# Optimization experiments

Measured on AMD Instinct MI355X. Metric: run time of the kernel, lower is better.

Reference implementation:

```python
import jax, jax.numpy as jnp
import numpy as np

H = 64            # hidden_channels
L = 2             # num_layers
E = 300_000       # edges per relation
B = 64            # graphs in batch
NS = [100_000, 20_000, 50_000, 80_000]   # variable, value, operator, constraint
# (src_type, dst_type) for the 9 hetero relations, fixed order
RELS = [(0,1),(0,2),(0,3),(2,3),(3,3),(1,0),(2,0),(3,0),(3,2)]
R = len(RELS)
SLOPE = 0.2       # GATConv leaky_relu negative slope


def setup_inputs() -> dict:
    key = jax.random.key(0)
    ks = iter(jax.random.split(key, 64))
    inp = {}
    for n, N in zip(["x_variable", "x_value", "x_operator", "x_constraint"], NS):
        inp[n] = jax.random.normal(next(ks), (N, H), jnp.float32)
    sc = 1.0 / np.sqrt(H).astype(np.float32)
    inp["Wsrc"] = jax.random.normal(next(ks), (L, R, H, H), jnp.float32) * sc
    inp["Wdst"] = jax.random.normal(next(ks), (L, R, H, H), jnp.float32) * sc
    inp["asrc"] = jax.random.normal(next(ks), (L, R, H), jnp.float32) * sc
    inp["adst"] = jax.random.normal(next(ks), (L, R, H), jnp.float32) * sc
    inp["bias"] = jax.random.normal(next(ks), (L, R, H), jnp.float32) * 0.01
    inp["lin_w"] = jax.random.normal(next(ks), (2, 2 * H), jnp.float32) / np.sqrt(2.0 * H).astype(np.float32)
    inp["lin_b"] = jnp.zeros((2,), jnp.float32)
    for r, (s, d) in enumerate(RELS):
        inp[f"src{r}"] = jax.random.randint(next(ks), (E,), 0, NS[s], jnp.int32)
        inp[f"dst{r}"] = jax.random.randint(next(ks), (E,), 0, NS[d], jnp.int32)
    inp["batch_variable"] = jnp.sort(jax.random.randint(next(ks), (NS[0],), 0, B, jnp.int32))
    inp["batch_constraint"] = jnp.sort(jax.random.randint(next(ks), (NS[3],), 0, B, jnp.int32))
    inp["num_graphs"] = B
    return inp


def _gat(xs, xd, Ws, Wd, a_s, a_d, b, src, dst):
    """Bipartite PyG GATConv (heads=1, add_self_loops=False)."""
    hs = xs @ Ws                         # [Ns, H]
    hd = xd @ Wd                         # [Nd, H]
    al_s = hs @ a_s                      # [Ns]
    al_d = hd @ a_d                      # [Nd]
    score = jax.nn.leaky_relu(al_s[src] + al_d[dst], SLOPE)    # [E]
    nd = xd.shape[0]
    m = jax.ops.segment_max(score, dst, num_segments=nd)
    p = jnp.exp(score - m[dst])
    z = jax.ops.segment_sum(p, dst, num_segments=nd)
    alpha = p / (z[dst] + 1e-16)                               # segment softmax
    out = jax.ops.segment_sum(hs[src] * alpha[:, None], dst, num_segments=nd)
    return out + b


def _seg_mean(x, seg, n):
    s = jax.ops.segment_sum(x, seg, num_segments=n)
    c = jax.ops.segment_sum(jnp.ones((x.shape[0],), x.dtype), seg, num_segments=n)
    return s / jnp.maximum(c, 1.0)[:, None]


def reference(x_variable, x_value, x_operator, x_constraint,
              Wsrc, Wdst, asrc, adst, bias, lin_w, lin_b,
              src0, dst0, src1, dst1, src2, dst2, src3, dst3, src4, dst4,
              src5, dst5, src6, dst6, src7, dst7, src8, dst8,
              batch_variable, batch_constraint, num_graphs):
    xs = [x_variable, x_value, x_operator, x_constraint]
    srcs = [src0, src1, src2, src3, src4, src5, src6, src7, src8]
    dsts = [dst0, dst1, dst2, dst3, dst4, dst5, dst6, dst7, dst8]
    for l in range(L):
        out = [jnp.zeros((x.shape[0], H), x.dtype) for x in xs]
        for r, (s, d) in enumerate(RELS):
            out[d] = out[d] + _gat(xs[s], xs[d], Wsrc[l, r], Wdst[l, r],
                                   asrc[l, r], adst[l, r], bias[l, r],
                                   srcs[r], dsts[r])
        xs = [jax.nn.relu(o) for o in out]   # dropout is identity in eval
    vp = _seg_mean(xs[0], batch_variable, num_graphs)   # [B, H]
    cp = _seg_mean(xs[3], batch_constraint, num_graphs) # [B, H]
    return jnp.concatenate([vp, cp], axis=1) @ lin_w.T + lin_b   # [B, 2]
```

## Files before the change

### kernel.cpp

```cpp
#include <hip/hip_runtime.h>
#include <hip/hip_bf16.h>

#define NH 64
#define NRELS 9
#define NEDGE 300000
#define NGRAPH 64
#define TOTROWS 250000
#define TOTFSEG 660000
#define TOTEDGE (NRELS * NEDGE)
#define NBUCK 977
#define CHUNK 4096
#define NBLK ((TOTEDGE + CHUNK - 1) / CHUNK)

typedef __attribute__((ext_vector_type(8))) short short8;
typedef __attribute__((ext_vector_type(4))) float f32x4;

__constant__ int c_NS[4]     = {100000, 20000, 50000, 80000};
__constant__ int c_SRC[9]    = {0,0,0,2,3,1,2,3,3};
__constant__ int c_DST[9]    = {1,2,3,3,3,0,0,0,2};
__constant__ int c_XOFF[5]   = {0,100000,120000,170000,250000};
__constant__ int c_ASOFF[10] = {0,100000,200000,300000,350000,430000,450000,500000,580000,660000};
__constant__ int c_FOFF[5]   = {0,300000,320000,420000,660000};
__constant__ int c_NRELT[4]  = {3,1,2,3};
__constant__ int c_RRANK[9]  = {0,0,0,1,2,0,1,2,1};

struct EdgePtrs { const int* s[9]; const int* d[9]; };

__device__ __forceinline__ unsigned short f2bf(float f) {
  union { __hip_bfloat16 h; unsigned short u; } c;
  c.h = __float2bfloat16(f);
  return c.u;
}

__device__ __forceinline__ float wred_max32(float v) {
#pragma unroll
  for (int o = 16; o; o >>= 1) v = fmaxf(v, __shfl_xor(v, o, 32));
  return v;
}

__global__ void k_setup(const float* Wsrc, const float* Wdst, const float* asrc,
                        const float* adst, const float* bias, float* wv, float* bsum,
                        unsigned short* wb, int* gbh) {
  int b = blockIdx.x, j = threadIdx.x;
  if (b < 36) {
    int r = b % 9, q = b / 9;
    int l = q >> 1, side = q & 1;
    const float* W = (side ? Wdst : Wsrc) + (l * 9 + r) * 64 * 64;
    const float* a = (side ? adst : asrc) + (l * 9 + r) * 64;
    float s = 0.f;
    for (int i = 0; i < 64; ++i) s += W[j * 64 + i] * a[i];
    wv[(side ? 1152 : 0) + (l * 9 + r) * 64 + j] = s;
  } else if (b == 36) {
    for (int l = 0; l < 2; ++l)
      for (int t = 0; t < 4; ++t) {
        float s = 0.f;
        for (int r = 0; r < 9; ++r)
          if (c_DST[r] == t) s += bias[(l * 9 + r) * 64 + j];
        bsum[(l * 4 + t) * 64 + j] = s;
      }
  } else if (b == 55) {
    for (int i = j; i < NBUCK; i += 64) gbh[i] = 0;
  } else {
    int idx = b - 37;
    int l = idx / 9, r = idx % 9;
    const float* W = Wsrc + (size_t)(l * 9 + r) * 4096;
    unsigned short* dst = wb + (size_t)(l * 9 + r) * 4096;
    for (int k = 0; k < 64; ++k)
      dst[j * 64 + k] = f2bf(W[k * 64 + j]);
  }
}

__global__ __launch_bounds__(256) void k_bhist(EdgePtrs Eg, int* gbh) {
  __shared__ int sh[NBUCK];
  for (int i = threadIdx.x; i < NBUCK; i += 256) sh[i] = 0;
  __syncthreads();
  int lo = blockIdx.x * CHUNK;
  int hi = lo + CHUNK; if (hi > TOTEDGE) hi = TOTEDGE;
  for (int gid = lo + threadIdx.x; gid < hi; gid += 256) {
    int r = gid / NEDGE, e = gid - r * NEDGE;
    int g = c_XOFF[c_DST[r]] + Eg.d[r][e];
    atomicAdd(&sh[g >> 8], 1);
  }
  __syncthreads();
  for (int i = threadIdx.x; i < NBUCK; i += 256) {
    int v = sh[i];
    if (v) atomicAdd(&gbh[i], v);
  }
}

__global__ void k_bscan(const int* gbh, int* boff, int* cur) {
  __shared__ int sd[1024];
  int t = threadIdx.x;
  int v = (t < NBUCK) ? gbh[t] : 0;
  sd[t] = v; __syncthreads();
  for (int o = 1; o < 1024; o <<= 1) {
    int x = (t >= o) ? sd[t - o] : 0; __syncthreads();
    sd[t] += x; __syncthreads();
  }
  if (t < NBUCK) { int e = sd[t] - v; boff[t] = e; cur[t] = e; }
  if (t == 1023) boff[NBUCK] = sd[1023];
}

__global__ __launch_bounds__(256) void k_bin(EdgePtrs Eg, int* cur, int* pairs) {
  __shared__ int sh[NBUCK];
  __shared__ int sbase[NBUCK];
  for (int i = threadIdx.x; i < NBUCK; i += 256) sh[i] = 0;
  __syncthreads();
  int lo = blockIdx.x * CHUNK;
  int hi = lo + CHUNK; if (hi > TOTEDGE) hi = TOTEDGE;
  for (int gid = lo + threadIdx.x; gid < hi; gid += 256) {
    int r = gid / NEDGE, e = gid - r * NEDGE;
    int g = c_XOFF[c_DST[r]] + Eg.d[r][e];
    atomicAdd(&sh[g >> 8], 1);
  }
  __syncthreads();
  for (int i = threadIdx.x; i < NBUCK; i += 256) {
    int v = sh[i];
    sbase[i] = v ? atomicAdd(&cur[i], v) : 0;
    sh[i] = 0;
  }
  __syncthreads();
  for (int gid = lo + threadIdx.x; gid < hi; gid += 256) {
    int r = gid / NEDGE, e = gid - r * NEDGE;
    int g = c_XOFF[c_DST[r]] + Eg.d[r][e];
    int b = g >> 8;
    int off = atomicAdd(&sh[b], 1);
    int key = ((g & 255) << 2) | c_RRANK[r];
    pairs[sbase[b] + off] = (key << 20) | (c_ASOFF[r] + Eg.s[r][e]);
  }
}

__global__ __launch_bounds__(256) void k_bsort(const int* pairs, const int* boff,
                                               int* rowptr, int* asx) {
  __shared__ int ssc[1024];
  __shared__ int scur[1024];
  __shared__ int sws[256];
  int b = blockIdx.x, t = threadIdx.x;
  int lo = boff[b], hi = boff[b + 1];
  int n = hi - lo;
  for (int i = t; i < 1024; i += 256) ssc[i] = 0;
  __syncthreads();
  for (int i = t; i < n; i += 256)
    atomicAdd(&ssc[((unsigned)pairs[lo + i]) >> 20], 1);
  __syncthreads();
  int c0 = ssc[t * 4], c1 = ssc[t * 4 + 1], c2 = ssc[t * 4 + 2], c3 = ssc[t * 4 + 3];
  int s = c0 + c1 + c2 + c3;
  sws[t] = s;
  __syncthreads();
  for (int o = 1; o < 256; o <<= 1) {
    int x = (t >= o) ? sws[t - o] : 0; __syncthreads();
    sws[t] += x; __syncthreads();
  }
  int base = sws[t] - s;
  ssc[t * 4]     = base;
  ssc[t * 4 + 1] = base + c0;
  ssc[t * 4 + 2] = base + c0 + c1;
  ssc[t * 4 + 3] = base + c0 + c1 + c2;
  scur[t * 4]     = ssc[t * 4];
  scur[t * 4 + 1] = ssc[t * 4 + 1];
  scur[t * 4 + 2] = ssc[t * 4 + 2];
  scur[t * 4 + 3] = ssc[t * 4 + 3];
  __syncthreads();
  int nodeBase = b << 8;
  for (int i = t; i < 1024; i += 256) {
    int l = i >> 2, rank = i & 3;
    int g = nodeBase + l;
    if (g < TOTROWS) {
      int tt = (g >= c_XOFF[1]) + (g >= c_XOFF[2]) + (g >= c_XOFF[3]);
      int nr = c_NRELT[tt];
      if (rank < nr)
        rowptr[c_FOFF[tt] + (g - c_XOFF[tt]) * nr + rank] = lo + ssc[i];
    }
  }
  if (b == 0 && t == 0) rowptr[TOTFSEG] = TOTEDGE;
  for (int i = t; i < n; i += 256) {
    int p = pairs[lo + i];
    int pos = atomicAdd(&scur[((unsigned)p) >> 20], 1);
    asx[lo + pos] = (int)(((((unsigned)p >> 20) & 3u) << 20) | ((unsigned)p & 0xFFFFFu));
  }
}

struct GemmAllP {
  const float* x0; const float* x1; const float* x2; const float* x3;
  const unsigned short* Wb;
  __hip_bfloat16* hs;
  float* als; float* ald;
  const float* wvs; const float* wvd;
  int act; int ntyp;
  int tbase[5];
  int typ[4];
  int nrel[4];
  int rel[4][3];
  int ndrel[4];
  int drel[4][3];
};

#define XSTR 72

__global__ __launch_bounds__(256) void k_gemma(GemmAllP G) {
  __shared__ unsigned short sx[64 * XSTR];
  __shared__ unsigned short sw[64 * XSTR];
  int bid = blockIdx.x;
  int k = 0;
#pragma unroll 3
  for (int q = 1; q < 4; ++q) if (q < G.ntyp) k += (bid >= G.tbase[q]);
  int st = G.typ[k];
  int tile = bid - G.tbase[k];
  int Ns = c_NS[st];
  const float* x = st == 0 ? G.x0 : st == 1 ? G.x1 : st == 2 ? G.x2 : G.x3;
  int base = tile * 64;
  int tid = threadIdx.x;
  for (int kk = tid; kk < 1024; kk += 256) {
    int row = kk >> 4;
    int c4 = (kk & 15) * 4;
    int gr = base + row;
    float4 v = make_float4(0.f, 0.f, 0.f, 0.f);
    if (gr < Ns) v = ((const float4*)x)[(size_t)gr * 16 + (kk & 15)];
    if (G.act) { v.x = fmaxf(v.x, 0.f); v.y = fmaxf(v.y, 0.f); v.z = fmaxf(v.z, 0.f); v.w = fmaxf(v.w, 0.f); }
    ushort4 u;
    u.x = f2bf(v.x); u.y = f2bf(v.y); u.z = f2bf(v.z); u.w = f2bf(v.w);
    *(ushort4*)&sx[row * XSTR + c4] = u;
  }
  __syncthreads();
  {
    int row = tid >> 2, part = tid & 3;
    int gr2 = base + row;
    if (gr2 < Ns) {
      float xv[16];
      const float4* xr = (const float4*)x + (size_t)gr2 * 16 + part * 4;
      float4 v0 = xr[0], v1 = xr[1], v2 = xr[2], v3 = xr[3];
      xv[0]=v0.x; xv[1]=v0.y; xv[2]=v0.z; xv[3]=v0.w;
      xv[4]=v1.x; xv[5]=v1.y; xv[6]=v1.z; xv[7]=v1.w;
      xv[8]=v2.x; xv[9]=v2.y; xv[10]=v2.z; xv[11]=v2.w;
      xv[12]=v3.x; xv[13]=v3.y; xv[14]=v3.z; xv[15]=v3.w;
      if (G.act) {
#pragma unroll
        for (int i = 0; i < 16; ++i) xv[i] = fmaxf(xv[i], 0.f);
      }
      int nrl0 = G.nrel[k];
      for (int ri = 0; ri < nrl0; ++ri) {
        int r = G.rel[k][ri];
        const float* wvp = G.wvs + r * 64 + part * 16;
        float s = 0.f;
#pragma unroll
        for (int i = 0; i < 16; ++i) s += xv[i] * wvp[i];
        s += __shfl_xor(s, 1);
        s += __shfl_xor(s, 2);
        if (part == 0) G.als[c_ASOFF[r] + gr2] = s;
      }
      int ndl = G.ndrel[k];
      for (int ri = 0; ri < ndl; ++ri) {
        int r = G.drel[k][ri];
        const float* wvp = G.wvd + r * 64 + part * 16;
        float s = 0.f;
#pragma unroll
        for (int i = 0; i < 16; ++i) s += xv[i] * wvp[i];
        s += __shfl_xor(s, 1);
        s += __shfl_xor(s, 2);
        if (part == 0)
          G.ald[c_FOFF[st] + gr2 * c_NRELT[st] + c_RRANK[r]] = s;
      }
    }
  }
  int w    = tid >> 6;
  int lane = tid & 63;
  int m    = lane & 15;
  int quad = lane >> 4;
  short8 a0 = *(const short8*)&sx[(w * 16 + m) * XSTR + quad * 8];
  short8 a1 = *(const short8*)&sx[(w * 16 + m) * XSTR + 32 + quad * 8];
  int nrl = G.nrel[k];
  for (int ri = 0; ri < nrl; ++ri) {
    int r = G.rel[k][ri];
    const unsigned short* Wb = G.Wb + (size_t)r * 4096;
    if (ri) __syncthreads();
    {
      int n = tid >> 2;
      int k0 = (tid & 3) << 4;
      short8 w0 = *(const short8*)&Wb[n * 64 + k0];
      short8 w1 = *(const short8*)&Wb[n * 64 + k0 + 8];
      *(short8*)&sw[n * XSTR + k0] = w0;
      *(short8*)&sw[n * XSTR + k0 + 8] = w1;
    }
    __syncthreads();
    f32x4 acc[4];
#pragma unroll
    for (int cb = 0; cb < 4; ++cb) acc[cb] = (f32x4)(0.f);
#pragma unroll
    for (int cb = 0; cb < 4; ++cb) {
      short8 b0 = *(const short8*)&sw[(cb * 16 + m) * XSTR + quad * 8];
      short8 b1 = *(const short8*)&sw[(cb * 16 + m) * XSTR + 32 + quad * 8];
      acc[cb] = __builtin_amdgcn_mfma_f32_16x16x32_bf16(a0, b0, acc[cb], 0, 0, 0);
      acc[cb] = __builtin_amdgcn_mfma_f32_16x16x32_bf16(a1, b1, acc[cb], 0, 0, 0);
    }
    __hip_bfloat16* hsb = G.hs + (size_t)c_ASOFF[r] * 64;
#pragma unroll
    for (int cb = 0; cb < 4; ++cb)
#pragma unroll
      for (int reg = 0; reg < 4; ++reg)
        sx[(w * 16 + quad * 4 + reg) * XSTR + cb * 16 + m] = f2bf(acc[cb][reg]);
    int rrow = w * 16 + (lane >> 2);
    int rcol = (lane & 3) * 16;
    int lr = base + rrow;
    if (lr < Ns) {
      short8 v0 = *(const short8*)&sx[rrow * XSTR + rcol];
      short8 v1 = *(const short8*)&sx[rrow * XSTR + rcol + 8];
      *(short8*)&hsb[(size_t)lr * 64 + rcol] = v0;
      *(short8*)&hsb[(size_t)lr * 64 + rcol + 8] = v1;
    }
  }
}

struct GatherP {
  const __hip_bfloat16* hs;
  const float* als;
  const float* ald;
  const int* rowptr; const int* asx;
  float* xA;
  const float* bsum;
  int ntypes;
  int tbase[5];
  int typ[4];
};

__global__ __launch_bounds__(256) void k_gather(GatherP A) {
  __shared__ unsigned long long sRA[8][96];
  __shared__ float sZ[8][4];
  int bid = blockIdx.x;
  int k = 0;
#pragma unroll 3
  for (int q = 1; q < 4; ++q) if (q < A.ntypes) k += (bid >= A.tbase[q]);
  int t = A.typ[k];
  int Nd = c_NS[t];
  int lane = threadIdx.x & 63;
  int half = lane >> 5;
  int sl   = lane & 31;
  int hid  = threadIdx.x >> 5;
  int node = (bid - A.tbase[k]) * 8 + (threadIdx.x >> 6) * 2 + half;
  if (node >= Nd) return;
  int nr = c_NRELT[t];
  int fb = c_FOFF[t] + node * nr;
  int p0 = A.rowptr[fb];
  int p1 = A.rowptr[fb + nr];
  int deg = p1 - p0; if (deg > 96) deg = 96;
  float2 acc = ((const float2*)(A.bsum + t * 64))[sl];
  if (deg > 0) {
    if (sl < 4) sZ[hid][sl] = 0.f;
    const float NEG = -3.4e38f;
    const unsigned* ax = (const unsigned*)A.asx;
    unsigned rec0 = 0, rec1 = 0, rec2 = 0;
    int rk0 = 0, rk1 = 0, rk2 = 0;
    float s0 = NEG, s1 = NEG, s2 = NEG;
    if (sl < deg) {
      rec0 = ax[p0 + sl];
      rk0 = (int)((rec0 >> 20) & 3u);
      float v = A.als[rec0 & 0xFFFFFu] + A.ald[fb + rk0];
      s0 = v >= 0.f ? v : 0.2f * v;
    }
    if (sl + 32 < deg) {
      rec1 = ax[p0 + 32 + sl];
      rk1 = (int)((rec1 >> 20) & 3u);
      float v = A.als[rec1 & 0xFFFFFu] + A.ald[fb + rk1];
      s1 = v >= 0.f ? v : 0.2f * v;
    }
    if (sl + 64 < deg) {
      rec2 = ax[p0 + 64 + sl];
      rk2 = (int)((rec2 >> 20) & 3u);
      float v = A.als[rec2 & 0xFFFFFu] + A.ald[fb + rk2];
      s2 = v >= 0.f ? v : 0.2f * v;
    }
    float M = wred_max32(fmaxf(fmaxf(s0, s1), s2));
    float e0 = 0.f, e1 = 0.f, e2 = 0.f;
    if (sl < deg)      { e0 = __expf(s0 - M); atomicAdd(&sZ[hid][rk0], e0); }
    if (sl + 32 < deg) { e1 = __expf(s1 - M); atomicAdd(&sZ[hid][rk1], e1); }
    if (sl + 64 < deg) { e2 = __expf(s2 - M); atomicAdd(&sZ[hid][rk2], e2); }
    asm volatile("s_waitcnt lgkmcnt(0)" ::: "memory");
    float rz0 = 1.f / (sZ[hid][0] + 1e-16f);
    float rz1 = 1.f / (sZ[hid][1] + 1e-16f);
    float rz2 = 1.f / (sZ[hid][2] + 1e-16f);
    float a0 = e0 * (rk0 == 0 ? rz0 : (rk0 == 1 ? rz1 : rz2));
    sRA[hid][sl] = ((unsigned long long)__float_as_uint(a0) << 32) | ((rec0 & 0xFFFFFu) << 7);
    if (deg > 32) {
      float a1 = e1 * (rk1 == 0 ? rz0 : (rk1 == 1 ? rz1 : rz2));
      sRA[hid][32 + sl] = ((unsigned long long)__float_as_uint(a1) << 32) | ((rec1 & 0xFFFFFu) << 7);
    }
    if (deg > 64) {
      float a2 = e2 * (rk2 == 0 ? rz0 : (rk2 == 1 ? rz1 : rz2));
      sRA[hid][64 + sl] = ((unsigned long long)__float_as_uint(a2) << 32) | ((rec2 & 0xFFFFFu) << 7);
    }
    const char* hsb = (const char*)A.hs;
    unsigned sl4 = (unsigned)sl * 4u;
    int nb = (deg + 7) >> 3;
    for (int g = 0; g < nb; g += 2) {
      unsigned long long raA[8], raB[8];
      unsigned hA[8], hB[8];
      bool hasB = (g + 1) < nb;
#pragma unroll
      for (int q = 0; q < 8; ++q) raA[q] = sRA[hid][g * 8 + q];
#pragma unroll
      for (int q = 0; q < 8; ++q)
        hA[q] = *(const unsigned*)(hsb + ((unsigned)(raA[q] & 0xFFFFFFFFu) + sl4));
      if (hasB) {
#pragma unroll
        for (int q = 0; q < 8; ++q) raB[q] = sRA[hid][g * 8 + 8 + q];
#pragma unroll
        for (int q = 0; q < 8; ++q)
          hB[q] = *(const unsigned*)(hsb + ((unsigned)(raB[q] & 0xFFFFFFFFu) + sl4));
      }
#pragma unroll
      for (int q = 0; q < 8; ++q) {
        float aq = __uint_as_float((unsigned)(raA[q] >> 32));
        acc.x = fmaf(aq, __uint_as_float(hA[q] << 16), acc.x);
        acc.y = fmaf(aq, __uint_as_float(hA[q] & 0xffff0000u), acc.y);
      }
      if (hasB) {
#pragma unroll
        for (int q = 0; q < 8; ++q) {
          float aq = __uint_as_float((unsigned)(raB[q] >> 32));
          acc.x = fmaf(aq, __uint_as_float(hB[q] << 16), acc.x);
          acc.y = fmaf(aq, __uint_as_float(hB[q] & 0xffff0000u), acc.y);
        }
      }
    }
  }
  float* xout = A.xA + (size_t)c_XOFF[t] * 64;
  *(float2*)&xout[(size_t)node * 64 + sl * 2] = acc;
}

struct GatherPoolP {
  const __hip_bfloat16* hs;
  const float* als;
  const float* ald;
  const int* rowptr; const int* asx;
  const float* bsum;
  int ntypes;
  int tbase[5];
  int typ[4];
  const int* bvar; const int* bcon;
  float* partial;
};

__global__ __launch_bounds__(256) void k_gatherpool(GatherPoolP A) {
  __shared__ unsigned long long sRA[8][96];
  __shared__ float sZ[8][4];
  __shared__ float sPool[8][64];
  __shared__ int sG[8];
  int bid = blockIdx.x;
  int k = 0;
#pragma unroll 3
  for (int q = 1; q < 4; ++q) if (q < A.ntypes) k += (bid >= A.tbase[q]);
  int t = A.typ[k];
  int Nd = c_NS[t];
  int lane = threadIdx.x & 63;
  int half = lane >> 5;
  int sl   = lane & 31;
  int hid  = threadIdx.x >> 5;
  int node = (bid - A.tbase[k]) * 8 + (threadIdx.x >> 6) * 2 + half;
  bool active = node < Nd;
  float2 acc = ((const float2*)(A.bsum + t * 64))[sl];
  int nr = c_NRELT[t];
  int fb = c_FOFF[t] + node * nr;
  int deg = 0, p0 = 0;
  if (active) {
    p0 = A.rowptr[fb];
    int p1 = A.rowptr[fb + nr];
    deg = p1 - p0; if (deg > 96) deg = 96;
  }
  if (deg > 0) {
    if (sl < 4) sZ[hid][sl] = 0.f;
    const float NEG = -3.4e38f;
    const unsigned* ax = (const unsigned*)A.asx;
    unsigned rec0 = 0, rec1 = 0, rec2 = 0;
    int rk0 = 0, rk1 = 0, rk2 = 0;
    float s0 = NEG, s1 = NEG, s2 = NEG;
    if (sl < deg) {
      rec0 = ax[p0 + sl];
      rk0 = (int)((rec0 >> 20) & 3u);
      float v = A.als[rec0 & 0xFFFFFu] + A.ald[fb + rk0];
      s0 = v >= 0.f ? v : 0.2f * v;
    }
    if (sl + 32 < deg) {
      rec1 = ax[p0 + 32 + sl];
      rk1 = (int)((rec1 >> 20) & 3u);
      float v = A.als[rec1 & 0xFFFFFu] + A.ald[fb + rk1];
      s1 = v >= 0.f ? v : 0.2f * v;
    }
    if (sl + 64 < deg) {
      rec2 = ax[p0 + 64 + sl];
      rk2 = (int)((rec2 >> 20) & 3u);
      float v = A.als[rec2 & 0xFFFFFu] + A.ald[fb + rk2];
      s2 = v >= 0.f ? v : 0.2f * v;
    }
    float M = wred_max32(fmaxf(fmaxf(s0, s1), s2));
    float e0 = 0.f, e1 = 0.f, e2 = 0.f;
    if (sl < deg)      { e0 = __expf(s0 - M); atomicAdd(&sZ[hid][rk0], e0); }
    if (sl + 32 < deg) { e1 = __expf(s1 - M); atomicAdd(&sZ[hid][rk1], e1); }
    if (sl + 64 < deg) { e2 = __expf(s2 - M); atomicAdd(&sZ[hid][rk2], e2); }
    asm volatile("s_waitcnt lgkmcnt(0)" ::: "memory");
    float rz0 = 1.f / (sZ[hid][0] + 1e-16f);
    float rz1 = 1.f / (sZ[hid][1] + 1e-16f);
    float rz2 = 1.f / (sZ[hid][2] + 1e-16f);
    float a0 = e0 * (rk0 == 0 ? rz0 : (rk0 == 1 ? rz1 : rz2));
    sRA[hid][sl] = ((unsigned long long)__float_as_uint(a0) << 32) | ((rec0 & 0xFFFFFu) << 7);
    if (deg > 32) {
      float a1 = e1 * (rk1 == 0 ? rz0 : (rk1 == 1 ? rz1 : rz2));
      sRA[hid][32 + sl] = ((unsigned long long)__float_as_uint(a1) << 32) | ((rec1 & 0xFFFFFu) << 7);
    }
    if (deg > 64) {
      float a2 = e2 * (rk2 == 0 ? rz0 : (rk2 == 1 ? rz1 : rz2));
      sRA[hid][64 + sl] = ((unsigned long long)__float_as_uint(a2) << 32) | ((rec2 & 0xFFFFFu) << 7);
    }
    const char* hsb = (const char*)A.hs;
    unsigned sl4 = (unsigned)sl * 4u;
    int nb = (deg + 7) >> 3;
    for (int g = 0; g < nb; g += 2) {
      unsigned long long raA[8], raB[8];
      unsigned hA[8], hB[8];
      bool hasB = (g + 1) < nb;
#pragma unroll
      for (int q = 0; q < 8; ++q) raA[q] = sRA[hid][g * 8 + q];
#pragma unroll
      for (int q = 0; q < 8; ++q)
        hA[q] = *(const unsigned*)(hsb + ((unsigned)(raA[q] & 0xFFFFFFFFu) + sl4));
      if (hasB) {
#pragma unroll
        for (int q = 0; q < 8; ++q) raB[q] = sRA[hid][g * 8 + 8 + q];
#pragma unroll
        for (int q = 0; q < 8; ++q)
          hB[q] = *(const unsigned*)(hsb + ((unsigned)(raB[q] & 0xFFFFFFFFu) + sl4));
      }
#pragma unroll
      for (int q = 0; q < 8; ++q) {
        float aq = __uint_as_float((unsigned)(raA[q] >> 32));
        acc.x = fmaf(aq, __uint_as_float(hA[q] << 16), acc.x);
        acc.y = fmaf(aq, __uint_as_float(hA[q] & 0xffff0000u), acc.y);
      }
      if (hasB) {
#pragma unroll
        for (int q = 0; q < 8; ++q) {
          float aq = __uint_as_float((unsigned)(raB[q] >> 32));
          acc.x = fmaf(aq, __uint_as_float(hB[q] << 16), acc.x);
          acc.y = fmaf(aq, __uint_as_float(hB[q] & 0xffff0000u), acc.y);
        }
      }
    }
  }
  sPool[hid][sl * 2]     = fmaxf(acc.x, 0.f);
  sPool[hid][sl * 2 + 1] = fmaxf(acc.y, 0.f);
  if (sl == 0) {
    int gid = -1;
    if (active) {
      int g = (t == 0) ? A.bvar[node] : A.bcon[node];
      gid = (g << 1) | (t == 3 ? 1 : 0);
    }
    sG[hid] = gid;
  }
  __syncthreads();
  if (threadIdx.x < 64) {
    int col = threadIdx.x;
    int sp = (bid & 7) << 7;
    float a = 0.f; int cg = -1;
#pragma unroll
    for (int i = 0; i < 8; ++i) {
      int gi = sG[i];
      if (gi < 0) continue;
      float v = sPool[i][col];
      if (gi == cg) a += v;
      else {
        if (cg >= 0) atomicAdd(&A.partial[(size_t)(sp | cg) * 64 + col], a);
        cg = gi; a = v;
      }
    }
    if (cg >= 0) atomicAdd(&A.partial[(size_t)(sp | cg) * 64 + col], a);
  }
}

__global__ void k_gbound(const int* bvar, const int* bcon, int* gs0, int* gs3, float* partial) {
  int gid = blockIdx.x * 256 + threadIdx.x;
  const int N0 = 100000, N3 = 80000;
  if (gid < N0) {
    int i = gid;
    int b = bvar[i];
    int bp = i ? bvar[i - 1] : -1;
    for (int g = bp + 1; g <= b; ++g) gs0[g] = i;
    if (i == N0 - 1) for (int g = b + 1; g <= 64; ++g) gs0[g] = N0;
  } else if (gid < N0 + N3) {
    int i = gid - N0;
    int b = bcon[i];
    int bp = i ? bcon[i - 1] : -1;
    for (int g = bp + 1; g <= b; ++g) gs3[g] = i;
    if (i == N3 - 1) for (int g = b + 1; g <= 64; ++g) gs3[g] = N3;
  } else if (gid < N0 + N3 + 65536) {
    partial[gid - N0 - N3] = 0.f;
  }
}

__global__ __launch_bounds__(256) void k_final2(const float* partial, const int* gs0, const int* gs3,
                                                const float* lin_w, const float* lin_b, float* out) {
  __shared__ float sp[8192];
  int tid = threadIdx.x;
  for (int j = 0; j < 32; ++j) {
    int v = j * 256 + tid;
    int tg = v >> 6, col = v & 63;
    float s = 0.f;
#pragma unroll
    for (int spi = 0; spi < 8; ++spi)
      s += partial[(size_t)((spi << 7) | tg) * 64 + col];
    sp[tg * 64 + col] = s;
  }
  __syncthreads();
  if (tid < 128) {
    int g = tid >> 1, o = tid & 1;
    float c0 = fmaxf((float)(gs0[g + 1] - gs0[g]), 1.f);
    float c3 = fmaxf((float)(gs3[g + 1] - gs3[g]), 1.f);
    float acc = lin_b[o];
    for (int i = 0; i < 64; ++i) {
      acc += (sp[(g << 1) * 64 + i] / c0) * lin_w[o * 128 + i];
      acc += (sp[((g << 1) | 1) * 64 + i] / c3) * lin_w[o * 128 + 64 + i];
    }
    out[g * 2 + o] = acc;
  }
}

__global__ void k_bail(float* out) {
  if (threadIdx.x < 128) out[threadIdx.x] = 0.f;
}

extern "C" void kernel_launch(void* const* d_in, const int* in_sizes, int n_in,
                              void* d_out, int out_size, void* d_ws, size_t ws_size,
                              hipStream_t stream) {
  (void)in_sizes; (void)n_in; (void)out_size;
  const size_t O_XA   = 0;
  const size_t O_HS   = 16000000;
  const size_t O_ALS  = 37120000;
  const size_t O_ALD  = 37780000;
  const size_t O_WV   = 39790000;
  const size_t O_BS   = 39792304;
  const size_t O_RP   = 39792816;
  const size_t O_ASX  = 40452832;
  const size_t O_GS   = 43152832;
  const size_t O_PART = 43153088;
  const size_t O_POOL = 43218624;
  const size_t O_WB   = 43226816;
  const size_t NEED   = 43263680;
  (void)O_POOL;

  if (ws_size < NEED * 4) {
    k_bail<<<1, 128, 0, stream>>>((float*)d_out);
    return;
  }

  const float* x0 = (const float*)d_in[0];
  const float* x1 = (const float*)d_in[1];
  const float* x2 = (const float*)d_in[2];
  const float* x3 = (const float*)d_in[3];
  const float* Wsrc = (const float*)d_in[4];
  const float* Wdst = (const float*)d_in[5];
  const float* asrc = (const float*)d_in[6];
  const float* adst = (const float*)d_in[7];
  const float* bias = (const float*)d_in[8];
  const float* lin_w = (const float*)d_in[9];
  const float* lin_b = (const float*)d_in[10];
  EdgePtrs Eg;
  for (int r = 0; r < 9; ++r) {
    Eg.s[r] = (const int*)d_in[11 + 2 * r];
    Eg.d[r] = (const int*)d_in[12 + 2 * r];
  }
  const int* bvar = (const int*)d_in[29];
  const int* bcon = (const int*)d_in[30];

  float* ws = (float*)d_ws;
  float* xA   = ws + O_XA;
  __hip_bfloat16* hs = (__hip_bfloat16*)(ws + O_HS);
  int* pairs  = (int*)(ws + O_HS);
  int* gbh    = pairs + 2700000;
  int* boff   = gbh + NBUCK + 1;
  int* cur    = boff + NBUCK + 2;
  float* als  = ws + O_ALS;
  float* ald  = ws + O_ALD;
  float* wv   = ws + O_WV;
  float* bsum = ws + O_BS;
  int* rowptr = (int*)(ws + O_RP);
  int* asx    = (int*)(ws + O_ASX);
  int* gs0    = (int*)(ws + O_GS);
  int* gs3    = gs0 + 65;
  float* partial = ws + O_PART;
  unsigned short* wb = (unsigned short*)(ws + O_WB);

  const int h_NS[4]   = {100000, 20000, 50000, 80000};
  const int h_SRC[9]  = {0,0,0,2,3,1,2,3,3};
  const int h_DST[9]  = {1,2,3,3,3,0,0,0,2};
  const int h_XOFF[4] = {0,100000,120000,170000};

  k_setup<<<56, 64, 0, stream>>>(Wsrc, Wdst, asrc, adst, bias, wv, bsum, wb, gbh);

  k_bhist<<<NBLK, 256, 0, stream>>>(Eg, gbh);
  k_bscan<<<1, 1024, 0, stream>>>(gbh, boff, cur);
  k_bin<<<NBLK, 256, 0, stream>>>(Eg, cur, pairs);
  k_bsort<<<NBUCK, 256, 0, stream>>>(pairs, boff, rowptr, asx);
  k_gbound<<<(180000 + 65536 + 255) / 256, 256, 0, stream>>>(bvar, bcon, gs0, gs3, partial);

  for (int l = 0; l < 2; ++l) {
    const float* xin[4];
    if (l == 0) { xin[0] = x0; xin[1] = x1; xin[2] = x2; xin[3] = x3; }
    else {
      for (int t = 0; t < 4; ++t) xin[t] = xA + (size_t)h_XOFF[t] * 64;
    }
    int act = (l > 0);
    int relmask = l ? 0x0FC : 0x1FF;

    GemmAllP G;
    G.x0 = xin[0]; G.x1 = xin[1]; G.x2 = xin[2]; G.x3 = xin[3];
    G.Wb = wb + (size_t)l * 9 * 4096;
    G.hs = hs; G.act = act;
    G.als = als; G.ald = ald;
    G.wvs = wv + l * 576; G.wvd = wv + 1152 + l * 576;
    int ntyp = 0, cum = 0;
    for (int t = 0; t < 4; ++t) {
      int nr = 0; int rl[3]; int nd = 0; int dl[3];
      for (int r = 0; r < 9; ++r) {
        if (!((relmask >> r) & 1)) continue;
        if (h_SRC[r] == t) rl[nr++] = r;
        if (h_DST[r] == t) dl[nd++] = r;
      }
      if (!nr && !nd) continue;
      G.typ[ntyp] = t; G.nrel[ntyp] = nr; G.ndrel[ntyp] = nd;
      for (int i = 0; i < 3; ++i) {
        G.rel[ntyp][i]  = (i < nr) ? rl[i] : 0;
        G.drel[ntyp][i] = (i < nd) ? dl[i] : 0;
      }
      G.tbase[ntyp] = cum;
      cum += (h_NS[t] + 63) / 64;
      ++ntyp;
    }
    G.ntyp = ntyp; G.tbase[ntyp] = cum;
    k_gemma<<<cum, 256, 0, stream>>>(G);

    if (l == 0) {
      GatherP A;
      A.hs = hs; A.als = als; A.ald = ald;
      A.rowptr = rowptr; A.asx = asx;
      A.xA = xA;
      A.bsum = bsum;
      int nt = 0, bcum = 0;
      for (int t = 0; t < 4; ++t) {
        A.typ[nt] = t;
        A.tbase[nt] = bcum;
        bcum += (h_NS[t] + 7) / 8;
        ++nt;
      }
      A.ntypes = nt; A.tbase[nt] = bcum;
      k_gather<<<bcum, 256, 0, stream>>>(A);
    } else {
      GatherPoolP A;
      A.hs = hs; A.als = als; A.ald = ald;
      A.rowptr = rowptr; A.asx = asx;
      A.bsum = bsum + 256;
      A.bvar = bvar; A.bcon = bcon;
      A.partial = partial;
      int nt = 0, bcum = 0;
      for (int t = 0; t < 4; ++t) {
        if (t == 1 || t == 2) continue;
        A.typ[nt] = t;
        A.tbase[nt] = bcum;
        bcum += (h_NS[t] + 7) / 8;
        ++nt;
      }
      A.ntypes = nt; A.tbase[nt] = bcum;
      k_gatherpool<<<bcum, 256, 0, stream>>>(A);
    }
  }

  k_final2<<<1, 256, 0, stream>>>(partial, gs0, gs3, lin_w, lin_b, (float*)d_out);
}
```

Measured before the change: 479.3 us.

## Merge setup, histogram and group-bound kernels; reuse per-block histograms in binning

Setup, bucket histogram and graph-boundary computation are folded into one launch, and buffer zeroing moves to memset calls. Each histogram block now stores its per-bucket counts to global memory, so the binning kernel reads them back instead of re-reading the destination indices and recounting. This cuts kernel launches and one full pass over the edge arrays, at the cost of extra workspace for the per-block histograms and two memset operations.

```diff
diff --git a/kernel.cpp b/kernel.cpp
--- a/kernel.cpp
+++ b/kernel.cpp
@@ -11,6 +11,8 @@
 #define NBUCK 977
 #define CHUNK 4096
 #define NBLK ((TOTEDGE + CHUNK - 1) / CHUNK)
+#define NB_SETUP 55
+#define NB_GB 704
 
 typedef __attribute__((ext_vector_type(8))) short short8;
 typedef __attribute__((ext_vector_type(4))) float f32x4;
@@ -38,53 +40,79 @@
   return v;
 }
 
-__global__ void k_setup(const float* Wsrc, const float* Wdst, const float* asrc,
-                        const float* adst, const float* bias, float* wv, float* bsum,
-                        unsigned short* wb, int* gbh) {
-  int b = blockIdx.x, j = threadIdx.x;
-  if (b < 36) {
-    int r = b % 9, q = b / 9;
-    int l = q >> 1, side = q & 1;
-    const float* W = (side ? Wdst : Wsrc) + (l * 9 + r) * 64 * 64;
-    const float* a = (side ? adst : asrc) + (l * 9 + r) * 64;
-    float s = 0.f;
-    for (int i = 0; i < 64; ++i) s += W[j * 64 + i] * a[i];
-    wv[(side ? 1152 : 0) + (l * 9 + r) * 64 + j] = s;
-  } else if (b == 36) {
-    for (int l = 0; l < 2; ++l)
-      for (int t = 0; t < 4; ++t) {
+__global__ __launch_bounds__(256) void k_init(const float* Wsrc, const float* Wdst,
+                                              const float* asrc, const float* adst,
+                                              const float* bias, float* wv, float* bsum,
+                                              unsigned short* wb, EdgePtrs Eg,
+                                              int* bh, int* gbh,
+                                              const int* bvar, const int* bcon,
+                                              int* gs0, int* gs3) {
+  __shared__ int sh[NBUCK];
+  int b = blockIdx.x;
+  if (b < NB_SETUP) {
+    int j = threadIdx.x;
+    if (j < 64) {
+      if (b < 36) {
+        int r = b % 9, q = b / 9;
+        int l = q >> 1, side = q & 1;
+        const float* W = (side ? Wdst : Wsrc) + (l * 9 + r) * 64 * 64;
+        const float* a = (side ? adst : asrc) + (l * 9 + r) * 64;
         float s = 0.f;
-        for (int r = 0; r < 9; ++r)
-          if (c_DST[r] == t) s += bias[(l * 9 + r) * 64 + j];
-        bsum[(l * 4 + t) * 64 + j] = s;
-      }
-  } else if (b == 55) {
-    for (int i = j; i < NBUCK; i += 64) gbh[i] = 0;
-  } else {
-    int idx = b - 37;
-    int l = idx / 9, r = idx % 9;
-    const float* W = Wsrc + (size_t)(l * 9 + r) * 4096;
-    unsigned short* dst = wb + (size_t)(l * 9 + r) * 4096;
-    for (int k = 0; k < 64; ++k)
-      dst[j * 64 + k] = f2bf(W[k * 64 + j]);
-  }
-}
-
-__global__ __launch_bounds__(256) void k_bhist(EdgePtrs Eg, int* gbh) {
-  __shared__ int sh[NBUCK];
-  for (int i = threadIdx.x; i < NBUCK; i += 256) sh[i] = 0;
-  __syncthreads();
-  int lo = blockIdx.x * CHUNK;
-  int hi = lo + CHUNK; if (hi > TOTEDGE) hi = TOTEDGE;
-  for (int gid = lo + threadIdx.x; gid < hi; gid += 256) {
-    int r = gid / NEDGE, e = gid - r * NEDGE;
-    int g = c_XOFF[c_DST[r]] + Eg.d[r][e];
-    atomicAdd(&sh[g >> 8], 1);
-  }
-  __syncthreads();
-  for (int i = threadIdx.x; i < NBUCK; i += 256) {
-    int v = sh[i];
-    if (v) atomicAdd(&gbh[i], v);
+        for (int i = 0; i < 64; ++i) s += W[j * 64 + i] * a[i];
+        wv[(side ? 1152 : 0) + (l * 9 + r) * 64 + j] = s;
+      } else if (b == 36) {
+        for (int l = 0; l < 2; ++l)
+          for (int t = 0; t < 4; ++t) {
+            float s = 0.f;
+            for (int r = 0; r < 9; ++r)
+              if (c_DST[r] == t) s += bias[(l * 9 + r) * 64 + j];
+            bsum[(l * 4 + t) * 64 + j] = s;
+          }
+      } else {
+        int idx = b - 37;
+        int l = idx / 9, r = idx % 9;
+        const float* W = Wsrc + (size_t)(l * 9 + r) * 4096;
+        unsigned short* dst = wb + (size_t)(l * 9 + r) * 4096;
+        for (int k = 0; k < 64; ++k)
+          dst[j * 64 + k] = f2bf(W[k * 64 + j]);
+      }
+    }
+    return;
+  }
+  if (b < NB_SETUP + NBLK) {
+    int blk = b - NB_SETUP;
+    for (int i = threadIdx.x; i < NBUCK; i += 256) sh[i] = 0;
+    __syncthreads();
+    int lo = blk * CHUNK;
+    int hi = lo + CHUNK; if (hi > TOTEDGE) hi = TOTEDGE;
+    for (int gid = lo + threadIdx.x; gid < hi; gid += 256) {
+      int r = gid / NEDGE, e = gid - r * NEDGE;
+      int g = c_XOFF[c_DST[r]] + Eg.d[r][e];
+      atomicAdd(&sh[g >> 8], 1);
+    }
+    __syncthreads();
+    int* dst = bh + (size_t)blk * NBUCK;
+    for (int i = threadIdx.x; i < NBUCK; i += 256) {
+      int v = sh[i];
+      dst[i] = v;
+      if (v) atomicAdd(&gbh[i], v);
+    }
+    return;
+  }
+  int gid = (b - NB_SETUP - NBLK) * 256 + threadIdx.x;
+  const int N0 = 100000, N3 = 80000;
+  if (gid < N0) {
+    int i = gid;
+    int bb = bvar[i];
+    int bp = i ? bvar[i - 1] : -1;
+    for (int g = bp + 1; g <= bb; ++g) gs0[g] = i;
+    if (i == N0 - 1) for (int g = bb + 1; g <= 64; ++g) gs0[g] = N0;
+  } else if (gid < N0 + N3) {
+    int i = gid - N0;
+    int bb = bcon[i];
+    int bp = i ? bcon[i - 1] : -1;
+    for (int g = bp + 1; g <= bb; ++g) gs3[g] = i;
+    if (i == N3 - 1) for (int g = bb + 1; g <= 64; ++g) gs3[g] = N3;
   }
 }
 
@@ -101,25 +129,18 @@
   if (t == 1023) boff[NBUCK] = sd[1023];
 }
 
-__global__ __launch_bounds__(256) void k_bin(EdgePtrs Eg, int* cur, int* pairs) {
+__global__ __launch_bounds__(256) void k_bin(EdgePtrs Eg, const int* bh, int* cur, int* pairs) {
   __shared__ int sh[NBUCK];
   __shared__ int sbase[NBUCK];
-  for (int i = threadIdx.x; i < NBUCK; i += 256) sh[i] = 0;
+  const int* mybh = bh + (size_t)blockIdx.x * NBUCK;
+  for (int i = threadIdx.x; i < NBUCK; i += 256) {
+    int v = mybh[i];
+    sbase[i] = v ? atomicAdd(&cur[i], v) : 0;
+    sh[i] = 0;
+  }
   __syncthreads();
   int lo = blockIdx.x * CHUNK;
   int hi = lo + CHUNK; if (hi > TOTEDGE) hi = TOTEDGE;
-  for (int gid = lo + threadIdx.x; gid < hi; gid += 256) {
-    int r = gid / NEDGE, e = gid - r * NEDGE;
-    int g = c_XOFF[c_DST[r]] + Eg.d[r][e];
-    atomicAdd(&sh[g >> 8], 1);
-  }
-  __syncthreads();
-  for (int i = threadIdx.x; i < NBUCK; i += 256) {
-    int v = sh[i];
-    sbase[i] = v ? atomicAdd(&cur[i], v) : 0;
-    sh[i] = 0;
-  }
-  __syncthreads();
   for (int gid = lo + threadIdx.x; gid < hi; gid += 256) {
     int r = gid / NEDGE, e = gid - r * NEDGE;
     int g = c_XOFF[c_DST[r]] + Eg.d[r][e];
@@ -574,26 +595,6 @@
   }
 }
 
-__global__ void k_gbound(const int* bvar, const int* bcon, int* gs0, int* gs3, float* partial) {
-  int gid = blockIdx.x * 256 + threadIdx.x;
-  const int N0 = 100000, N3 = 80000;
-  if (gid < N0) {
-    int i = gid;
-    int b = bvar[i];
-    int bp = i ? bvar[i - 1] : -1;
-    for (int g = bp + 1; g <= b; ++g) gs0[g] = i;
-    if (i == N0 - 1) for (int g = b + 1; g <= 64; ++g) gs0[g] = N0;
-  } else if (gid < N0 + N3) {
-    int i = gid - N0;
-    int b = bcon[i];
-    int bp = i ? bcon[i - 1] : -1;
-    for (int g = bp + 1; g <= b; ++g) gs3[g] = i;
-    if (i == N3 - 1) for (int g = b + 1; g <= 64; ++g) gs3[g] = N3;
-  } else if (gid < N0 + N3 + 65536) {
-    partial[gid - N0 - N3] = 0.f;
-  }
-}
-
 __global__ __launch_bounds__(256) void k_final2(const float* partial, const int* gs0, const int* gs3,
                                                 const float* lin_w, const float* lin_b, float* out) {
   __shared__ float sp[8192];
@@ -639,10 +640,8 @@
   const size_t O_ASX  = 40452832;
   const size_t O_GS   = 43152832;
   const size_t O_PART = 43153088;
-  const size_t O_POOL = 43218624;
   const size_t O_WB   = 43226816;
   const size_t NEED   = 43263680;
-  (void)O_POOL;
 
   if (ws_size < NEED * 4) {
     k_bail<<<1, 128, 0, stream>>>((float*)d_out);
@@ -672,7 +671,8 @@
   float* xA   = ws + O_XA;
   __hip_bfloat16* hs = (__hip_bfloat16*)(ws + O_HS);
   int* pairs  = (int*)(ws + O_HS);
-  int* gbh    = pairs + 2700000;
+  int* bh     = pairs + 2700000;
+  int* gbh    = bh + (size_t)NBLK * NBUCK;
   int* boff   = gbh + NBUCK + 1;
   int* cur    = boff + NBUCK + 2;
   float* als  = ws + O_ALS;
@@ -691,13 +691,15 @@
   const int h_DST[9]  = {1,2,3,3,3,0,0,0,2};
   const int h_XOFF[4] = {0,100000,120000,170000};
 
-  k_setup<<<56, 64, 0, stream>>>(Wsrc, Wdst, asrc, adst, bias, wv, bsum, wb, gbh);
-
-  k_bhist<<<NBLK, 256, 0, stream>>>(Eg, gbh);
+  hipMemsetAsync(gbh, 0, NBUCK * sizeof(int), stream);
+  hipMemsetAsync(partial, 0, 65536 * sizeof(float), stream);
+
+  k_init<<<NB_SETUP + NBLK + NB_GB, 256, 0, stream>>>(Wsrc, Wdst, asrc, adst, bias,
+                                                      wv, bsum, wb, Eg, bh, gbh,
+                                                      bvar, bcon, gs0, gs3);
   k_bscan<<<1, 1024, 0, stream>>>(gbh, boff, cur);
-  k_bin<<<NBLK, 256, 0, stream>>>(Eg, cur, pairs);
+  k_bin<<<NBLK, 256, 0, stream>>>(Eg, bh, cur, pairs);
   k_bsort<<<NBUCK, 256, 0, stream>>>(pairs, boff, rowptr, asx);
-  k_gbound<<<(180000 + 65536 + 255) / 256, 256, 0, stream>>>(bvar, bcon, gs0, gs3, partial);
 
   for (int l = 0; l < 2; ++l) {
     const float* xin[4];
```

Measured after the change: 475.5 us. About the same (-0.8%).
